# Kernel optimization log

Hardware: AMD Instinct MI355X
Metric: run time of the kernel (lower is better)

The kernel has to match this reference:

```python
import jax, jax.numpy as jnp
import numpy as np

B, T, C, H, HS = 128, 256, 384, 6, 64

def setup_inputs() -> dict:
    key = jax.random.key(0)
    k1, k2, k3, k4, k5 = jax.random.split(key, 5)
    s = 0.02
    return {
        "x": jax.random.normal(k1, (B, T, C), dtype=jnp.float32),
        "Wq": jax.random.normal(k2, (H, C, HS), dtype=jnp.float32) * s,
        "Wk": jax.random.normal(k3, (H, C, HS), dtype=jnp.float32) * s,
        "Wv": jax.random.normal(k4, (H, C, HS), dtype=jnp.float32) * s,
        "Wp": jax.random.normal(k5, (C, C), dtype=jnp.float32) * s,
        "bp": jnp.zeros((C,), dtype=jnp.float32),
    }

def reference(x, Wq, Wk, Wv, Wp, bp):
    # per-head projections: [B,H,T,HS]
    q = jnp.einsum('btc,hcd->bhtd', x, Wq)
    k = jnp.einsum('btc,hcd->bhtd', x, Wk)
    v = jnp.einsum('btc,hcd->bhtd', x, Wv)
    scale = 1.0 / jnp.sqrt(jnp.asarray(HS, dtype=x.dtype))
    # scores: [B,H,T,T], causal mask then stable softmax
    scores = jnp.einsum('bhtd,bhsd->bhts', q, k) * scale
    causal = jnp.tril(jnp.ones((T, T), dtype=bool))
    scores = jnp.where(causal, scores, -jnp.inf)
    wei = jax.nn.softmax(scores, axis=-1)
    # dropout is identity in eval mode
    out = jnp.einsum('bhts,bhsd->bhtd', wei, v)  # [B,H,T,HS]
    out = out.transpose(0, 2, 1, 3).reshape(B, T, H * HS)  # concat heads
    return out @ Wp.T + bp  # output projection
```

## Files before the change

kernel.cpp:

```cpp
#include <hip/hip_runtime.h>
#include <hip/hip_bf16.h>
#include <math.h>

#define B_   128
#define T_   256
#define C_   384
#define H_   6
#define HS_  64
#define NTOK (B_*T_)
#define NQKV (3*C_)

typedef unsigned short u16;
typedef __attribute__((ext_vector_type(8))) short bf16x8;
typedef __attribute__((ext_vector_type(4))) float f32x4;

__device__ __forceinline__ u16 f2b(float f) {
    unsigned int u = __builtin_bit_cast(unsigned int, f);
    unsigned int r = (u + 0x7FFFu + ((u >> 16) & 1u)) >> 16;
    return (u16)r;
}

__device__ __forceinline__ float fexp2(float x) {
#if __has_builtin(__builtin_amdgcn_exp2f)
    return __builtin_amdgcn_exp2f(x);
#else
    return exp2f(x);
#endif
}

__device__ __forceinline__ void gl2lds16(const u16* g, u16* l) {
    __builtin_amdgcn_global_load_lds(
        (const __attribute__((address_space(1))) unsigned int*)g,
        (__attribute__((address_space(3))) unsigned int*)l, 16, 0, 0);
}

#define QSCALE 0.180336880f

#define J0_ (NTOK*C_/8)
#define J2_ (C_*C_/8)
#define J1_ (NQKV*C_)

__global__ __launch_bounds__(256) void prep(
    const float* __restrict__ x,  const float* __restrict__ Wq,
    const float* __restrict__ Wk, const float* __restrict__ Wv,
    const float* __restrict__ Wp,
    u16* __restrict__ xb, u16* __restrict__ wct, u16* __restrict__ wpb)
{
    int i = blockIdx.x * 256 + threadIdx.x;
    if (i < J0_) {
        const float4* s = (const float4*)x + (size_t)i * 2;
        float4 a = s[0], b = s[1];
        ushort4 o1, o2;
        o1.x = f2b(a.x); o1.y = f2b(a.y); o1.z = f2b(a.z); o1.w = f2b(a.w);
        o2.x = f2b(b.x); o2.y = f2b(b.y); o2.z = f2b(b.z); o2.w = f2b(b.w);
        ((ushort4*)xb)[(size_t)i * 2]     = o1;
        ((ushort4*)xb)[(size_t)i * 2 + 1] = o2;
    } else if (i < J0_ + J2_) {
        int j = i - J0_;
        const float4* s = (const float4*)Wp + (size_t)j * 2;
        float4 a = s[0], b = s[1];
        ushort4 o1, o2;
        o1.x = f2b(a.x); o1.y = f2b(a.y); o1.z = f2b(a.z); o1.w = f2b(a.w);
        o2.x = f2b(b.x); o2.y = f2b(b.y); o2.z = f2b(b.z); o2.w = f2b(b.w);
        ((ushort4*)wpb)[(size_t)j * 2]     = o1;
        ((ushort4*)wpb)[(size_t)j * 2 + 1] = o2;
    } else {
        int j = i - J0_ - J2_;
        if (j < J1_) {
            int n = j / C_, c = j % C_;
            int h = n / 192, rem = n % 192;
            int p = rem >> 6, d = rem & 63;
            const float* W = (p == 0 ? Wq : (p == 1 ? Wk : Wv));
            wct[j] = f2b(W[(h * C_ + c) * HS_ + d]);
        }
    }
}

__global__ __launch_bounds__(512, 2) void qkv_attn(
    const u16* __restrict__ xb, const u16* __restrict__ wct,
    u16* __restrict__ yb)
{
    __shared__ __align__(16) u16 SM[49152];
    u16* Qs = SM;
    u16* Ks = SM + 16384;
    u16* Vs = SM + 32768;

    const int gid = blockIdx.x;
    const int lin = (gid & 7) * 96 + (gid >> 3);
    const int b = lin / 6, h = lin % 6;

    const int tid = threadIdx.x;
    const int w = tid >> 6, lane = tid & 63;
    const int lm = lane & 15, qd = lane >> 4;
    const int wm = (w >> 1) * 64, wn = (w & 1) * 96;

    const int schunk = (lane & 7) ^ ((lane >> 3) & 7);
    const u16* gA = xb  + (size_t)(b * T_ + w * 32 + (lane >> 3)) * C_ + schunk * 8;
    const u16* gB = wct + (size_t)(h * 192 + w * 24 + (lane >> 3)) * C_ + schunk * 8;
    u16* lA = &Qs[(w * 32) * 64];
    u16* lB = &Ks[(w * 24) * 64];

    f32x4 acc[4][6];
    #pragma unroll
    for (int mi = 0; mi < 4; ++mi)
        #pragma unroll
        for (int ni = 0; ni < 6; ++ni)
            acc[mi][ni] = (f32x4){0.f, 0.f, 0.f, 0.f};

    for (int k0 = 0; k0 < C_; k0 += 64) {
        __syncthreads();
        #pragma unroll
        for (int j = 0; j < 4; ++j)
            gl2lds16(gA + j * 8 * C_, lA + j * 8 * 64);
        #pragma unroll
        for (int j = 0; j < 3; ++j)
            gl2lds16(gB + j * 8 * C_, lB + j * 8 * 64);
        gA += 64; gB += 64;
        __syncthreads();

        #pragma unroll
        for (int ks = 0; ks < 2; ++ks) {
            bf16x8 af[4], bfr[6];
            #pragma unroll
            for (int mi = 0; mi < 4; ++mi) {
                const int row = wm + mi * 16 + lm;
                const int sl = (ks * 4 + qd) ^ (lm & 7);
                af[mi] = *(const bf16x8*)&Qs[row * 64 + sl * 8];
            }
            #pragma unroll
            for (int ni = 0; ni < 6; ++ni) {
                const int row = wn + ni * 16 + lm;
                const int sl = (ks * 4 + qd) ^ (lm & 7);
                bfr[ni] = *(const bf16x8*)&Ks[row * 64 + sl * 8];
            }
            #pragma unroll
            for (int mi = 0; mi < 4; ++mi)
                #pragma unroll
                for (int ni = 0; ni < 6; ++ni)
                    acc[mi][ni] = __builtin_amdgcn_mfma_f32_16x16x32_bf16(
                        af[mi], bfr[ni], acc[mi][ni], 0, 0, 0);
        }
    }

    __syncthreads();
    #pragma unroll
    for (int mi = 0; mi < 4; ++mi) {
        const int t0 = wm + mi * 16 + qd * 4;
        #pragma unroll
        for (int ni = 0; ni < 6; ++ni) {
            const int n = wn + ni * 16 + lm;
            if (n < 64) {
                #pragma unroll
                for (int r = 0; r < 4; ++r) {
                    const int t = t0 + r;
                    Qs[t * 64 + (((n >> 3) ^ (t & 7)) << 3) + (n & 7)]
                        = f2b(acc[mi][ni][r] * QSCALE);
                }
            } else if (n < 128) {
                const int d = n - 64;
                #pragma unroll
                for (int r = 0; r < 4; ++r) {
                    const int t = t0 + r;
                    Ks[t * 64 + (((d >> 3) ^ (t & 7)) << 3) + (d & 7)]
                        = f2b(acc[mi][ni][r]);
                }
            } else {
                const int d = n - 128;
                const int ch = t0 >> 3;
                const int pos = (ch & 16) | ((ch ^ (d & 15)) & 15);
                ushort4 sv;
                sv.x = f2b(acc[mi][ni][0]); sv.y = f2b(acc[mi][ni][1]);
                sv.z = f2b(acc[mi][ni][2]); sv.w = f2b(acc[mi][ni][3]);
                *(ushort4*)&Vs[d * 256 + pos * 8 + (t0 & 7)] = sv;
            }
        }
    }
    __syncthreads();

    bf16x8 aq[2][2];
    #pragma unroll
    for (int rg = 0; rg < 2; ++rg) {
        const int t = rg * 128 + w * 16 + lm;
        #pragma unroll
        for (int ks = 0; ks < 2; ++ks)
            aq[rg][ks] = *(const bf16x8*)
                &Qs[t * 64 + (((ks * 4 + qd) ^ (t & 7)) << 3)];
    }
    __syncthreads();

    f32x4 oacc[2][4];
    float ms[2][4], ls[2][4];
    #pragma unroll
    for (int rg = 0; rg < 2; ++rg) {
        #pragma unroll
        for (int ni = 0; ni < 4; ++ni) oacc[rg][ni] = (f32x4){0.f, 0.f, 0.f, 0.f};
        #pragma unroll
        for (int r = 0; r < 4; ++r) { ms[rg][r] = -INFINITY; ls[rg][r] = 0.f; }
    }

    u16* Pw = SM + w * (16 * 72);

    #pragma unroll
    for (int rg = 0; rg < 2; ++rg) {
        const int trg = rg * 128 + w * 16;
        const int kmax = (trg + 15) >> 6;
        for (int kt = 0; kt <= kmax; ++kt) {
            const int j0 = kt * 64;
            const bool needmask = (j0 + 63 > trg);

            f32x4 st[4];
            #pragma unroll
            for (int ni = 0; ni < 4; ++ni) st[ni] = (f32x4){0.f, 0.f, 0.f, 0.f};
            #pragma unroll
            for (int ks = 0; ks < 2; ++ks) {
                #pragma unroll
                for (int ni = 0; ni < 4; ++ni) {
                    const int krow = j0 + ni * 16 + lm;
                    const int sl = (ks * 4 + qd) ^ (lm & 7);
                    bf16x8 bk = *(const bf16x8*)&Ks[krow * 64 + sl * 8];
                    st[ni] = __builtin_amdgcn_mfma_f32_16x16x32_bf16(
                        aq[rg][ks], bk, st[ni], 0, 0, 0);
                }
            }

            float vals[4][4], rowmax[4];
            #pragma unroll
            for (int r = 0; r < 4; ++r) rowmax[r] = -INFINITY;
            #pragma unroll
            for (int ni = 0; ni < 4; ++ni) {
                const int s_g = j0 + ni * 16 + lm;
                #pragma unroll
                for (int r = 0; r < 4; ++r) {
                    float sc = st[ni][r];
                    if (needmask) {
                        const int t_g = trg + qd * 4 + r;
                        sc = (s_g > t_g) ? -1e30f : sc;
                    }
                    vals[ni][r] = sc;
                    rowmax[r] = fmaxf(rowmax[r], sc);
                }
            }
            #pragma unroll
            for (int msk = 1; msk <= 8; msk <<= 1)
                #pragma unroll
                for (int r = 0; r < 4; ++r)
                    rowmax[r] = fmaxf(rowmax[r], __shfl_xor(rowmax[r], msk, 64));

            float corr[4], rowsum[4];
            #pragma unroll
            for (int r = 0; r < 4; ++r) {
                const float mn = fmaxf(ms[rg][r], rowmax[r]);
                corr[r] = fexp2(ms[rg][r] - mn);
                ms[rg][r] = mn;
                rowsum[r] = 0.f;
            }
            #pragma unroll
            for (int ni = 0; ni < 4; ++ni) {
                #pragma unroll
                for (int r = 0; r < 4; ++r) {
                    const float pv = fexp2(vals[ni][r] - ms[rg][r]);
                    rowsum[r] += pv;
                    Pw[(qd * 4 + r) * 72 + ni * 16 + lm] = f2b(pv);
                }
            }
            #pragma unroll
            for (int msk = 1; msk <= 8; msk <<= 1)
                #pragma unroll
                for (int r = 0; r < 4; ++r)
                    rowsum[r] += __shfl_xor(rowsum[r], msk, 64);
            #pragma unroll
            for (int r = 0; r < 4; ++r) ls[rg][r] = ls[rg][r] * corr[r] + rowsum[r];
            #pragma unroll
            for (int ni = 0; ni < 4; ++ni)
                #pragma unroll
                for (int r = 0; r < 4; ++r)
                    oacc[rg][ni][r] *= corr[r];

            #pragma unroll
            for (int ks = 0; ks < 2; ++ks) {
                bf16x8 pa = *(const bf16x8*)&Pw[lm * 72 + ks * 32 + qd * 8];
                #pragma unroll
                for (int ni = 0; ni < 4; ++ni) {
                    const int d = ni * 16 + lm;
                    const int cj = kt * 8 + ks * 4 + qd;
                    const int pos = (cj & 16) | ((cj ^ (d & 15)) & 15);
                    bf16x8 bv = *(const bf16x8*)&Vs[d * 256 + pos * 8];
                    oacc[rg][ni] = __builtin_amdgcn_mfma_f32_16x16x32_bf16(
                        pa, bv, oacc[rg][ni], 0, 0, 0);
                }
            }
        }
    }

    __syncthreads();
    u16 (*yt)[72] = (u16(*)[72])SM;
    #pragma unroll
    for (int rg = 0; rg < 2; ++rg) {
        const int trow = rg * 128 + w * 16 + qd * 4;
        #pragma unroll
        for (int r = 0; r < 4; ++r) {
            const float inv = 1.f / ls[rg][r];
            #pragma unroll
            for (int ni = 0; ni < 4; ++ni)
                yt[trow + r][ni * 16 + lm] = f2b(oacc[rg][ni][r] * inv);
        }
    }
    __syncthreads();
    #pragma unroll
    for (int rr = 0; rr < 4; ++rr) {
        const int row = rr * 64 + (tid >> 3);
        const int col = (tid & 7) * 8;
        bf16x8 vv = *(const bf16x8*)&yt[row][col];
        *(bf16x8*)(yb + ((size_t)(b * T_ + row)) * C_ + h * 64 + col) = vv;
    }
}

__global__ __launch_bounds__(512, 4) void gemm_proj(
    const u16* __restrict__ yb, const u16* __restrict__ wpb,
    const float* __restrict__ bp, float* __restrict__ out)
{
    __shared__ __align__(16) u16 SMEM[256 * 64 + 128 * 64];
    u16* As = SMEM;
    u16* Bs = SMEM + 256 * 64;

    const int gid  = blockIdx.x;
    const int xcd  = gid & 7;
    const int j_   = gid >> 3;
    const int colb = j_ % 3;
    const int rowb = (j_ / 3) * 8 + xcd;
    const int m0g  = rowb * 256;
    const int n0g  = colb * 128;

    const int tid = threadIdx.x;
    const int w = tid >> 6, lane = tid & 63;
    const int lm = lane & 15, qd = lane >> 4;
    const int wm = (w >> 1) * 64, wn = (w & 1) * 64;

    const int schunk = (lane & 7) ^ ((lane >> 3) & 7);
    const u16* gA = yb  + (size_t)(m0g + w * 32 + (lane >> 3)) * C_ + schunk * 8;
    const u16* gB = wpb + (size_t)(n0g + w * 16 + (lane >> 3)) * C_ + schunk * 8;
    u16* lA = &As[(w * 32) * 64];
    u16* lB = &Bs[(w * 16) * 64];

    f32x4 acc[4][4];
    #pragma unroll
    for (int mi = 0; mi < 4; ++mi)
        #pragma unroll
        for (int ni = 0; ni < 4; ++ni)
            acc[mi][ni] = (f32x4){0.f, 0.f, 0.f, 0.f};

    for (int k0 = 0; k0 < C_; k0 += 64) {
        __syncthreads();
        #pragma unroll
        for (int j = 0; j < 4; ++j)
            gl2lds16(gA + j * 8 * C_, lA + j * 8 * 64);
        #pragma unroll
        for (int j = 0; j < 2; ++j)
            gl2lds16(gB + j * 8 * C_, lB + j * 8 * 64);
        gA += 64; gB += 64;
        __syncthreads();

        #pragma unroll
        for (int ks = 0; ks < 2; ++ks) {
            bf16x8 af[4], bfr[4];
            #pragma unroll
            for (int mi = 0; mi < 4; ++mi) {
                const int row = wm + mi * 16 + lm;
                const int sl = (ks * 4 + qd) ^ (lm & 7);
                af[mi] = *(const bf16x8*)&As[row * 64 + sl * 8];
            }
            #pragma unroll
            for (int ni = 0; ni < 4; ++ni) {
                const int row = wn + ni * 16 + lm;
                const int sl = (ks * 4 + qd) ^ (lm & 7);
                bfr[ni] = *(const bf16x8*)&Bs[row * 64 + sl * 8];
            }
            #pragma unroll
            for (int mi = 0; mi < 4; ++mi)
                #pragma unroll
                for (int ni = 0; ni < 4; ++ni)
                    acc[mi][ni] = __builtin_amdgcn_mfma_f32_16x16x32_bf16(
                        af[mi], bfr[ni], acc[mi][ni], 0, 0, 0);
        }
    }

    float bpv[4];
    #pragma unroll
    for (int ni = 0; ni < 4; ++ni) bpv[ni] = bp[n0g + wn + ni * 16 + lm];

    float (*tb)[132] = (float(*)[132])SMEM;
    const int rloc = tid >> 3;
    #pragma unroll
    for (int mi = 0; mi < 4; ++mi) {
        __syncthreads();
        #pragma unroll
        for (int ni = 0; ni < 4; ++ni)
            #pragma unroll
            for (int r = 0; r < 4; ++r)
                tb[(w >> 1) * 16 + qd * 4 + r][wn + ni * 16 + lm]
                    = acc[mi][ni][r] + bpv[ni];
        __syncthreads();
        const int m = m0g + (rloc >> 4) * 64 + mi * 16 + (rloc & 15);
        #pragma unroll
        for (int jj = 0; jj < 4; ++jj) {
            const int cc = (tid & 7) * 4 + jj * 32;
            float4 vv = *(const float4*)&tb[rloc][cc];
            *(float4*)(out + (size_t)m * C_ + n0g + cc) = vv;
        }
    }
}

extern "C" void kernel_launch(void* const* d_in, const int* in_sizes, int n_in,
                              void* d_out, int out_size, void* d_ws, size_t ws_size,
                              hipStream_t stream)
{
    const float* x  = (const float*)d_in[0];
    const float* Wq = (const float*)d_in[1];
    const float* Wk = (const float*)d_in[2];
    const float* Wv = (const float*)d_in[3];
    const float* Wp = (const float*)d_in[4];
    const float* bp = (const float*)d_in[5];
    float* out = (float*)d_out;

    u16* xb  = (u16*)d_ws;
    u16* wct = xb  + (size_t)NTOK * C_;
    u16* wpb = wct + (size_t)NQKV * C_;
    u16* yb  = wpb + (size_t)C_ * C_;

    const int prep_blocks = (J0_ + J2_ + J1_ + 255) / 256;
    hipLaunchKernelGGL(prep, dim3(prep_blocks), dim3(256), 0, stream,
                       x, Wq, Wk, Wv, Wp, xb, wct, wpb);

    hipLaunchKernelGGL(qkv_attn, dim3(B_ * H_), dim3(512), 0, stream,
                       xb, wct, yb);

    hipLaunchKernelGGL(gemm_proj, dim3((NTOK / 256) * (C_ / 128)), dim3(512), 0, stream,
                       yb, wpb, bp, out);
}
```

Measured before the change: 187.9 us.

## Shrink attention LDS footprint by aliasing Q/K regions and rebalance causal rows

Cuts shared memory from 96KB to 80KB per block by staging Q through the K region: Q fragments are loaded into registers before K is written over them, V goes into the former x-tile region, and the P scratch uses a swizzled 64-wide layout instead of a padded 72-wide one. Launch bounds are raised from 2 to 4 blocks per CU to request higher occupancy, which pressures the register budget and may cause spills. The second row group per wave is mirrored (128+(7-w)*16) so each wave's total causal work is balanced across waves. An extra barrier and a second pass over the accumulators are added to write K after Q has been consumed.

```diff
diff --git a/kernel.cpp b/kernel.cpp
--- a/kernel.cpp
+++ b/kernel.cpp
@@ -76,14 +76,14 @@
     }
 }
 
-__global__ __launch_bounds__(512, 2) void qkv_attn(
+__global__ __launch_bounds__(512, 4) void qkv_attn(
     const u16* __restrict__ xb, const u16* __restrict__ wct,
     u16* __restrict__ yb)
 {
-    __shared__ __align__(16) u16 SM[49152];
-    u16* Qs = SM;
-    u16* Ks = SM + 16384;
-    u16* Vs = SM + 32768;
+    __shared__ __align__(16) u16 SM[40960];
+    u16* R0 = SM;
+    u16* R1 = SM + 16384;
+    u16* R2 = SM + 32768;
 
     const int gid = blockIdx.x;
     const int lin = (gid & 7) * 96 + (gid >> 3);
@@ -97,8 +97,8 @@
     const int schunk = (lane & 7) ^ ((lane >> 3) & 7);
     const u16* gA = xb  + (size_t)(b * T_ + w * 32 + (lane >> 3)) * C_ + schunk * 8;
     const u16* gB = wct + (size_t)(h * 192 + w * 24 + (lane >> 3)) * C_ + schunk * 8;
-    u16* lA = &Qs[(w * 32) * 64];
-    u16* lB = &Ks[(w * 24) * 64];
+    u16* lA = &R0[(w * 32) * 64];
+    u16* lB = &R1[(w * 24) * 64];
 
     f32x4 acc[4][6];
     #pragma unroll
@@ -125,13 +125,13 @@
             for (int mi = 0; mi < 4; ++mi) {
                 const int row = wm + mi * 16 + lm;
                 const int sl = (ks * 4 + qd) ^ (lm & 7);
-                af[mi] = *(const bf16x8*)&Qs[row * 64 + sl * 8];
+                af[mi] = *(const bf16x8*)&R0[row * 64 + sl * 8];
             }
             #pragma unroll
             for (int ni = 0; ni < 6; ++ni) {
                 const int row = wn + ni * 16 + lm;
                 const int sl = (ks * 4 + qd) ^ (lm & 7);
-                bfr[ni] = *(const bf16x8*)&Ks[row * 64 + sl * 8];
+                bfr[ni] = *(const bf16x8*)&R1[row * 64 + sl * 8];
             }
             #pragma unroll
             for (int mi = 0; mi < 4; ++mi)
@@ -153,38 +153,51 @@
                 #pragma unroll
                 for (int r = 0; r < 4; ++r) {
                     const int t = t0 + r;
-                    Qs[t * 64 + (((n >> 3) ^ (t & 7)) << 3) + (n & 7)]
+                    R1[t * 64 + (((n >> 3) ^ (t & 7)) << 3) + (n & 7)]
                         = f2b(acc[mi][ni][r] * QSCALE);
                 }
-            } else if (n < 128) {
-                const int d = n - 64;
-                #pragma unroll
-                for (int r = 0; r < 4; ++r) {
-                    const int t = t0 + r;
-                    Ks[t * 64 + (((d >> 3) ^ (t & 7)) << 3) + (d & 7)]
-                        = f2b(acc[mi][ni][r]);
-                }
-            } else {
+            } else if (n >= 128) {
                 const int d = n - 128;
                 const int ch = t0 >> 3;
                 const int pos = (ch & 16) | ((ch ^ (d & 15)) & 15);
                 ushort4 sv;
                 sv.x = f2b(acc[mi][ni][0]); sv.y = f2b(acc[mi][ni][1]);
                 sv.z = f2b(acc[mi][ni][2]); sv.w = f2b(acc[mi][ni][3]);
-                *(ushort4*)&Vs[d * 256 + pos * 8 + (t0 & 7)] = sv;
-            }
-        }
-    }
-    __syncthreads();
-
+                *(ushort4*)&R0[d * 256 + pos * 8 + (t0 & 7)] = sv;
+            }
+        }
+    }
+    __syncthreads();
+
+    const int trg0 = w * 16;
+    const int trg1 = 128 + (7 - w) * 16;
     bf16x8 aq[2][2];
     #pragma unroll
     for (int rg = 0; rg < 2; ++rg) {
-        const int t = rg * 128 + w * 16 + lm;
+        const int t = (rg ? trg1 : trg0) + lm;
         #pragma unroll
         for (int ks = 0; ks < 2; ++ks)
             aq[rg][ks] = *(const bf16x8*)
-                &Qs[t * 64 + (((ks * 4 + qd) ^ (t & 7)) << 3)];
+                &R1[t * 64 + (((ks * 4 + qd) ^ (t & 7)) << 3)];
+    }
+    __syncthreads();
+
+    #pragma unroll
+    for (int mi = 0; mi < 4; ++mi) {
+        const int t0 = wm + mi * 16 + qd * 4;
+        #pragma unroll
+        for (int ni = 0; ni < 6; ++ni) {
+            const int n = wn + ni * 16 + lm;
+            if (n >= 64 && n < 128) {
+                const int d = n - 64;
+                #pragma unroll
+                for (int r = 0; r < 4; ++r) {
+                    const int t = t0 + r;
+                    R1[t * 64 + (((d >> 3) ^ (t & 7)) << 3) + (d & 7)]
+                        = f2b(acc[mi][ni][r]);
+                }
+            }
+        }
     }
     __syncthreads();
 
@@ -198,11 +211,11 @@
         for (int r = 0; r < 4; ++r) { ms[rg][r] = -INFINITY; ls[rg][r] = 0.f; }
     }
 
-    u16* Pw = SM + w * (16 * 72);
+    u16* Pw = R2 + w * 1024;
 
     #pragma unroll
     for (int rg = 0; rg < 2; ++rg) {
-        const int trg = rg * 128 + w * 16;
+        const int trg = rg ? trg1 : trg0;
         const int kmax = (trg + 15) >> 6;
         for (int kt = 0; kt <= kmax; ++kt) {
             const int j0 = kt * 64;
@@ -217,7 +230,7 @@
                 for (int ni = 0; ni < 4; ++ni) {
                     const int krow = j0 + ni * 16 + lm;
                     const int sl = (ks * 4 + qd) ^ (lm & 7);
-                    bf16x8 bk = *(const bf16x8*)&Ks[krow * 64 + sl * 8];
+                    bf16x8 bk = *(const bf16x8*)&R1[krow * 64 + sl * 8];
                     st[ni] = __builtin_amdgcn_mfma_f32_16x16x32_bf16(
                         aq[rg][ks], bk, st[ni], 0, 0, 0);
                 }
@@ -260,7 +273,10 @@
                 for (int r = 0; r < 4; ++r) {
                     const float pv = fexp2(vals[ni][r] - ms[rg][r]);
                     rowsum[r] += pv;
-                    Pw[(qd * 4 + r) * 72 + ni * 16 + lm] = f2b(pv);
+                    const int prow = qd * 4 + r;
+                    const int pcol = ni * 16 + lm;
+                    const int pch  = (pcol >> 3) ^ (prow & 7);
+                    Pw[prow * 64 + pch * 8 + (pcol & 7)] = f2b(pv);
                 }
             }
             #pragma unroll
@@ -278,13 +294,14 @@
 
             #pragma unroll
             for (int ks = 0; ks < 2; ++ks) {
-                bf16x8 pa = *(const bf16x8*)&Pw[lm * 72 + ks * 32 + qd * 8];
+                const int rch = (ks * 4 + qd) ^ (lm & 7);
+                bf16x8 pa = *(const bf16x8*)&Pw[lm * 64 + rch * 8];
                 #pragma unroll
                 for (int ni = 0; ni < 4; ++ni) {
                     const int d = ni * 16 + lm;
                     const int cj = kt * 8 + ks * 4 + qd;
                     const int pos = (cj & 16) | ((cj ^ (d & 15)) & 15);
-                    bf16x8 bv = *(const bf16x8*)&Vs[d * 256 + pos * 8];
+                    bf16x8 bv = *(const bf16x8*)&R0[d * 256 + pos * 8];
                     oacc[rg][ni] = __builtin_amdgcn_mfma_f32_16x16x32_bf16(
                         pa, bv, oacc[rg][ni], 0, 0, 0);
                 }
@@ -296,7 +313,7 @@
     u16 (*yt)[72] = (u16(*)[72])SM;
     #pragma unroll
     for (int rg = 0; rg < 2; ++rg) {
-        const int trow = rg * 128 + w * 16 + qd * 4;
+        const int trow = (rg ? trg1 : trg0) + qd * 4;
         #pragma unroll
         for (int r = 0; r < 4; ++r) {
             const float inv = 1.f / ls[rg][r];
```

Result: slower. 283.2 us (+50.7%).
